# Kernel tuning notes

Hardware: AMD Instinct MI355X
Metric: run time of the kernel (lower is better)

## Reference

```python
import jax, jax.numpy as jnp
import numpy as np
import math

# Dims chosen per input_specs
B, Q, S, T = 8, 64, 64, 64          # batch, queries, stat (segment) count, tokens per segment
H, DH = 8, 64                        # heads, head dim
NH = H * DH                          # num_hiddens = 512
STAT_K, TOKEN_K = 8, 16
NEG = -1e6


def setup_inputs() -> dict:
    key = jax.random.key(0)
    ks = jax.random.split(key, 11)
    f = lambda k, sh: jax.random.normal(k, sh, dtype=jnp.float32)
    w = lambda k: f(k, (NH, NH)) * 0.05  # Linear weights stored as [in, out]
    return {
        "queries": f(ks[0], (B, Q, NH)),
        "stat_keys": f(ks[1], (B, S, NH)),
        "token_keys": f(ks[2], (B * S, T, NH)),
        "values": f(ks[3], (B * S, T, NH)),
        "stat_valid_lens": jax.random.randint(ks[4], (B,), 1, S + 1, dtype=jnp.int32),
        "Wq_stat": w(ks[5]),
        "Wq_token": w(ks[6]),
        "Wk_stat": w(ks[7]),
        "Wk_token": w(ks[8]),
        "Wv": w(ks[9]),
        "Wo": w(ks[10]),
    }


def reference(queries, stat_keys, token_keys, values, stat_valid_lens,
              Wq_stat, Wq_token, Wk_stat, Wk_token, Wv, Wo):
    scale = 1.0 / math.sqrt(DH)

    def split_heads(x):  # [b, L, H*DH] -> [b, H, L, DH]
        b, L, _ = x.shape
        return x.reshape(b, L, H, DH).transpose(0, 2, 1, 3)

    q_stat = split_heads(queries @ Wq_stat)        # [B,H,Q,DH]
    q_tok = split_heads(queries @ Wq_token)        # [B,H,Q,DH]
    k_stat = split_heads(stat_keys @ Wk_stat)      # [B,H,S,DH]
    # token_keys/values come in as [B*S, T, size]; per-head layout [B,H,S,T,DH]
    k_tok = (token_keys @ Wk_token).reshape(B, S, T, H, DH).transpose(0, 3, 1, 2, 4)
    v = (values @ Wv).reshape(B, S, T, H, DH).transpose(0, 3, 1, 2, 4)

    # --- stat-level scores, valid-length mask, top-k sparsification, softmax ---
    stat_scores = jnp.einsum('bhqd,bhsd->bhqs', q_stat, k_stat) * scale  # [B,H,Q,S]
    valid = jnp.arange(S)[None, None, None, :] < stat_valid_lens[:, None, None, None]
    stat_scores = jnp.where(valid, stat_scores, NEG)
    k1 = min(S - 1, STAT_K)
    _, top_idx = jax.lax.top_k(stat_scores, k1)                           # [B,H,Q,k1]
    keep = jax.nn.one_hot(top_idx, S, dtype=stat_scores.dtype).sum(-2) > 0  # [B,H,Q,S]
    stat_w = jax.nn.softmax(jnp.where(keep, stat_scores, NEG), axis=-1)   # [B,H,Q,S]

    # --- token-level scores. NOTE: the original code computes torch.topk but then
    # overwrites with the LAST k2 positions (token_weights[:, :, -k2:] = ...), so the
    # token top-k result is dead code; we faithfully reproduce the last-k2 masking. ---
    tok_scores = jnp.einsum('bhqd,bhstd->bhsqt', q_tok, k_tok) * scale    # [B,H,S,Q,T]
    k2 = min(T - 1, TOKEN_K)
    last_mask = jnp.arange(T) >= (T - k2)
    tok_w = jax.nn.softmax(jnp.where(last_mask, tok_scores, NEG), axis=-1)
    tok_w = tok_w.transpose(0, 1, 3, 2, 4)                                # [B,H,Q,S,T]

    # --- combine hierarchy and attend over values ---
    comb = stat_w[..., None] * tok_w                                      # [B,H,Q,S,T]
    out = jnp.einsum('bhqst,bhstd->bhqd', comb, v)                        # [B,H,Q,DH]
    out = out.transpose(0, 2, 1, 3).reshape(B, Q, NH)
    return out @ Wo
```

## Files before the change

### kernel.cpp

```cpp
#include <hip/hip_runtime.h>
#include <hip/hip_bf16.h>

#define BB 8
#define QQ 64
#define SS 64
#define TT 64
#define HH 8
#define DH 64
#define NHID 512
#define STAT_K 8
#define TOKEN_K 16

typedef short bf16x8 __attribute__((ext_vector_type(8)));
typedef float f32x4 __attribute__((ext_vector_type(4)));

__device__ inline ushort f2bf_rne(float x) {
    union { float f; unsigned u; } v; v.f = x;
    unsigned r = v.u + 0x7fff + ((v.u >> 16) & 1);
    return (ushort)(r >> 16);
}
__device__ inline float bf2f(ushort h) {
    union { unsigned u; float f; } v; v.u = ((unsigned)h) << 16;
    return v.f;
}

__global__ __launch_bounds__(256) void conv_w(
    const float* w0, const float* w1, const float* w2,
    const float* w3, const float* w4, const float* w5, ushort* wT)
{
    const int z = blockIdx.z;
    const float* srcs[6] = {w0, w1, w2, w3, w4, w5};
    const float* src = srcs[z];
    ushort* hi = wT + (size_t)z * 524288;
    ushort* lo = hi + 262144;
    __shared__ float t[32][33];
    const int c0 = blockIdx.x * 32, r0 = blockIdx.y * 32;
    const int tx = threadIdx.x & 31, ty = threadIdx.x >> 5;
    #pragma unroll
    for (int i = 0; i < 4; ++i)
        t[ty + 8 * i][tx] = src[(r0 + ty + 8 * i) * 512 + c0 + tx];
    __syncthreads();
    #pragma unroll
    for (int i = 0; i < 4; ++i) {
        float x = t[tx][ty + 8 * i];
        ushort h = f2bf_rne(x);
        int o = (c0 + ty + 8 * i) * 512 + r0 + tx;
        hi[o] = h;
        lo[o] = f2bf_rne(x - bf2f(h));
    }
}

__global__ __launch_bounds__(256) void gemm_split3(
    const float* __restrict__ queries, const float* __restrict__ stat_keys,
    const ushort* __restrict__ wT,
    float* __restrict__ q_stat, float* __restrict__ k_stat,
    float* __restrict__ q_tokf)
{
    const int z = blockIdx.z;
    const float* Afp = (z == 1) ? stat_keys : queries;
    const ushort* Bh = wT + (size_t)z * 524288;
    const ushort* Bl = Bh + 262144;
    float* C = (z == 0) ? q_stat : (z == 1) ? k_stat : q_tokf;
    const int K = 512, N = 512;

    __shared__ ushort As[2][64][40];
    __shared__ ushort Bs[2][64][40];
    const int tid = threadIdx.x;
    const int row0 = blockIdx.y * 64, col0 = blockIdx.x * 64;
    const int wave = tid >> 6, lane = tid & 63;
    const int wm = wave & 1, wn = wave >> 1;
    const int m16 = lane & 15, quad = lane >> 4;
    const int srow = tid >> 2, schunk = tid & 3;

    const float*  aptr  = Afp + (size_t)(row0 + srow) * K + schunk * 8;
    const ushort* bptrh = Bh + (size_t)(col0 + srow) * K + schunk * 8;
    const ushort* bptrl = Bl + (size_t)(col0 + srow) * K + schunk * 8;

    f32x4 acc[2][2];
    #pragma unroll
    for (int i = 0; i < 2; ++i)
        #pragma unroll
        for (int j = 0; j < 2; ++j)
            #pragma unroll
            for (int r = 0; r < 4; ++r) acc[i][j][r] = 0.f;

    for (int k0 = 0; k0 < K; k0 += 32) {
        float4 ax0 = ((const float4*)(aptr + k0))[0];
        float4 ax1 = ((const float4*)(aptr + k0))[1];
        uint4  bvh = *(const uint4*)(bptrh + k0);
        uint4  bvl = *(const uint4*)(bptrl + k0);
        ushort4 h0, h1, l0, l1;
        h0.x = f2bf_rne(ax0.x); l0.x = f2bf_rne(ax0.x - bf2f(h0.x));
        h0.y = f2bf_rne(ax0.y); l0.y = f2bf_rne(ax0.y - bf2f(h0.y));
        h0.z = f2bf_rne(ax0.z); l0.z = f2bf_rne(ax0.z - bf2f(h0.z));
        h0.w = f2bf_rne(ax0.w); l0.w = f2bf_rne(ax0.w - bf2f(h0.w));
        h1.x = f2bf_rne(ax1.x); l1.x = f2bf_rne(ax1.x - bf2f(h1.x));
        h1.y = f2bf_rne(ax1.y); l1.y = f2bf_rne(ax1.y - bf2f(h1.y));
        h1.z = f2bf_rne(ax1.z); l1.z = f2bf_rne(ax1.z - bf2f(h1.z));
        h1.w = f2bf_rne(ax1.w); l1.w = f2bf_rne(ax1.w - bf2f(h1.w));
        *(ushort4*)&As[0][srow][schunk * 8]     = h0;
        *(ushort4*)&As[0][srow][schunk * 8 + 4] = h1;
        *(ushort4*)&As[1][srow][schunk * 8]     = l0;
        *(ushort4*)&As[1][srow][schunk * 8 + 4] = l1;
        *(uint4*)&Bs[0][srow][schunk * 8] = bvh;
        *(uint4*)&Bs[1][srow][schunk * 8] = bvl;
        __syncthreads();

        bf16x8 af[2], bf[2], afl[2], bfl[2];
        #pragma unroll
        for (int i = 0; i < 2; ++i) {
            af[i]  = *(const bf16x8*)&As[0][wm * 32 + i * 16 + m16][quad * 8];
            bf[i]  = *(const bf16x8*)&Bs[0][wn * 32 + i * 16 + m16][quad * 8];
            afl[i] = *(const bf16x8*)&As[1][wm * 32 + i * 16 + m16][quad * 8];
            bfl[i] = *(const bf16x8*)&Bs[1][wn * 32 + i * 16 + m16][quad * 8];
        }
        #pragma unroll
        for (int i = 0; i < 2; ++i)
            #pragma unroll
            for (int j = 0; j < 2; ++j) {
                acc[i][j] = __builtin_amdgcn_mfma_f32_16x16x32_bf16(af[i], bf[j], acc[i][j], 0, 0, 0);
                acc[i][j] = __builtin_amdgcn_mfma_f32_16x16x32_bf16(af[i], bfl[j], acc[i][j], 0, 0, 0);
                acc[i][j] = __builtin_amdgcn_mfma_f32_16x16x32_bf16(afl[i], bf[j], acc[i][j], 0, 0, 0);
            }
        __syncthreads();
    }

    #pragma unroll
    for (int i = 0; i < 2; ++i)
        #pragma unroll
        for (int j = 0; j < 2; ++j) {
            int r0 = row0 + wm * 32 + i * 16 + quad * 4;
            int c = col0 + wn * 32 + j * 16 + m16;
            #pragma unroll
            for (int reg = 0; reg < 4; ++reg)
                C[(size_t)(r0 + reg) * N + c] = acc[i][j][reg];
        }
}

__global__ __launch_bounds__(256) void gemm_out(
    const ushort* __restrict__ Ah, const ushort* __restrict__ Al,
    const ushort* __restrict__ Bh, const ushort* __restrict__ Bl,
    float* __restrict__ C)
{
    const int K = 512, N = 512;
    __shared__ ushort As[2][64][40];
    __shared__ ushort Bs[2][64][40];
    const int tid = threadIdx.x;
    const int row0 = blockIdx.y * 64, col0 = blockIdx.x * 64;
    const int wave = tid >> 6, lane = tid & 63;
    const int wm = wave & 1, wn = wave >> 1;
    const int m16 = lane & 15, quad = lane >> 4;
    const int srow = tid >> 2, schunk = tid & 3;

    f32x4 acc[2][2];
    #pragma unroll
    for (int i = 0; i < 2; ++i)
        #pragma unroll
        for (int j = 0; j < 2; ++j)
            #pragma unroll
            for (int r = 0; r < 4; ++r) acc[i][j][r] = 0.f;

    for (int k0 = 0; k0 < K; k0 += 32) {
        const size_t aoff = (size_t)(row0 + srow) * K + k0 + schunk * 8;
        const size_t boff = (size_t)(col0 + srow) * K + k0 + schunk * 8;
        *(uint4*)&As[0][srow][schunk * 8] = *(const uint4*)(Ah + aoff);
        *(uint4*)&Bs[0][srow][schunk * 8] = *(const uint4*)(Bh + boff);
        *(uint4*)&As[1][srow][schunk * 8] = *(const uint4*)(Al + aoff);
        *(uint4*)&Bs[1][srow][schunk * 8] = *(const uint4*)(Bl + boff);
        __syncthreads();

        bf16x8 af[2], bf[2], afl[2], bfl[2];
        #pragma unroll
        for (int i = 0; i < 2; ++i) {
            af[i]  = *(const bf16x8*)&As[0][wm * 32 + i * 16 + m16][quad * 8];
            bf[i]  = *(const bf16x8*)&Bs[0][wn * 32 + i * 16 + m16][quad * 8];
            afl[i] = *(const bf16x8*)&As[1][wm * 32 + i * 16 + m16][quad * 8];
            bfl[i] = *(const bf16x8*)&Bs[1][wn * 32 + i * 16 + m16][quad * 8];
        }
        #pragma unroll
        for (int i = 0; i < 2; ++i)
            #pragma unroll
            for (int j = 0; j < 2; ++j) {
                acc[i][j] = __builtin_amdgcn_mfma_f32_16x16x32_bf16(af[i], bf[j], acc[i][j], 0, 0, 0);
                acc[i][j] = __builtin_amdgcn_mfma_f32_16x16x32_bf16(af[i], bfl[j], acc[i][j], 0, 0, 0);
                acc[i][j] = __builtin_amdgcn_mfma_f32_16x16x32_bf16(afl[i], bf[j], acc[i][j], 0, 0, 0);
            }
        __syncthreads();
    }

    #pragma unroll
    for (int i = 0; i < 2; ++i)
        #pragma unroll
        for (int j = 0; j < 2; ++j) {
            int r0 = row0 + wm * 32 + i * 16 + quad * 4;
            int c = col0 + wn * 32 + j * 16 + m16;
            #pragma unroll
            for (int reg = 0; reg < 4; ++reg)
                C[(size_t)(r0 + reg) * N + c] = acc[i][j][reg];
        }
}

__global__ __launch_bounds__(256) void gemm_tok(
    const float* __restrict__ token_keys, const ushort* __restrict__ wkt_h,
    ushort* __restrict__ k_tok)
{
    const int K = 512, N = 512;
    __shared__ ushort As[64][40];
    __shared__ ushort Bs[256][40];
    const int tid = threadIdx.x;
    const int row0 = blockIdx.y * 64, col0 = blockIdx.x * 256;
    const int wave = tid >> 6, lane = tid & 63;
    const int m16 = lane & 15, quad = lane >> 4;
    const int srow = tid >> 2, schunk = tid & 3;

    const int r = row0 + srow;
    const size_t arow = (size_t)((r >> 4) * 64 + 48 + (r & 15)) * K;

    f32x4 acc[4][4];
    #pragma unroll
    for (int i = 0; i < 4; ++i)
        #pragma unroll
        for (int j = 0; j < 4; ++j)
            #pragma unroll
            for (int rr = 0; rr < 4; ++rr) acc[i][j][rr] = 0.f;

    for (int k0 = 0; k0 < K; k0 += 32) {
        const float* ap = token_keys + arow + k0 + schunk * 8;
        float4 x0 = ((const float4*)ap)[0];
        float4 x1 = ((const float4*)ap)[1];
        ushort4 h0, h1;
        h0.x = f2bf_rne(x0.x); h0.y = f2bf_rne(x0.y);
        h0.z = f2bf_rne(x0.z); h0.w = f2bf_rne(x0.w);
        h1.x = f2bf_rne(x1.x); h1.y = f2bf_rne(x1.y);
        h1.z = f2bf_rne(x1.z); h1.w = f2bf_rne(x1.w);
        *(ushort4*)&As[srow][schunk * 8] = h0;
        *(ushort4*)&As[srow][schunk * 8 + 4] = h1;
        #pragma unroll
        for (int i = 0; i < 4; ++i) {
            int v = tid + i * 256;
            int brow = v >> 2, bchunk = v & 3;
            *(uint4*)&Bs[brow][bchunk * 8] =
                *(const uint4*)(wkt_h + (size_t)(col0 + brow) * K + k0 + bchunk * 8);
        }
        __syncthreads();

        bf16x8 af[4], bf[4];
        #pragma unroll
        for (int i = 0; i < 4; ++i) {
            af[i] = *(const bf16x8*)&As[i * 16 + m16][quad * 8];
            bf[i] = *(const bf16x8*)&Bs[wave * 64 + i * 16 + m16][quad * 8];
        }
        #pragma unroll
        for (int i = 0; i < 4; ++i)
            #pragma unroll
            for (int j = 0; j < 4; ++j)
                acc[i][j] = __builtin_amdgcn_mfma_f32_16x16x32_bf16(af[i], bf[j], acc[i][j], 0, 0, 0);
        __syncthreads();
    }

    #pragma unroll
    for (int i = 0; i < 4; ++i)
        #pragma unroll
        for (int j = 0; j < 4; ++j) {
            int r0 = row0 + i * 16 + quad * 4;
            int c = col0 + wave * 64 + j * 16 + m16;
            #pragma unroll
            for (int reg = 0; reg < 4; ++reg)
                k_tok[(size_t)(r0 + reg) * N + c] = f2bf_rne(acc[i][j][reg]);
        }
}

__global__ __launch_bounds__(256) void gemm_vT(
    const float* __restrict__ values, const ushort* __restrict__ wv_h,
    ushort* __restrict__ vT)
{
    const int K = 512;
    __shared__ ushort As[256][40];
    __shared__ ushort Bs[64][40];
    const int tid = threadIdx.x;
    const int row0m = blockIdx.y * 256, col0n = blockIdx.x * 64;
    const int wave = tid >> 6, lane = tid & 63;
    const int m16 = lane & 15, quad = lane >> 4;
    const int srow = tid >> 2, schunk = tid & 3;

    const int n = col0n + srow;
    const size_t brow = (size_t)((n >> 4) * 64 + 48 + (n & 15)) * K;

    f32x4 acc[4][4];
    #pragma unroll
    for (int i = 0; i < 4; ++i)
        #pragma unroll
        for (int j = 0; j < 4; ++j)
            #pragma unroll
            for (int rr = 0; rr < 4; ++rr) acc[i][j][rr] = 0.f;

    for (int k0 = 0; k0 < K; k0 += 32) {
        const float* bp = values + brow + k0 + schunk * 8;
        float4 x0 = ((const float4*)bp)[0];
        float4 x1 = ((const float4*)bp)[1];
        ushort4 h0, h1;
        h0.x = f2bf_rne(x0.x); h0.y = f2bf_rne(x0.y);
        h0.z = f2bf_rne(x0.z); h0.w = f2bf_rne(x0.w);
        h1.x = f2bf_rne(x1.x); h1.y = f2bf_rne(x1.y);
        h1.z = f2bf_rne(x1.z); h1.w = f2bf_rne(x1.w);
        *(ushort4*)&Bs[srow][schunk * 8] = h0;
        *(ushort4*)&Bs[srow][schunk * 8 + 4] = h1;
        #pragma unroll
        for (int i = 0; i < 4; ++i) {
            int v = tid + i * 256;
            int ar = v >> 2, ac = v & 3;
            *(uint4*)&As[ar][ac * 8] =
                *(const uint4*)(wv_h + (size_t)(row0m + ar) * K + k0 + ac * 8);
        }
        __syncthreads();

        bf16x8 af[4], bf[4];
        #pragma unroll
        for (int i = 0; i < 4; ++i) {
            af[i] = *(const bf16x8*)&As[wave * 64 + i * 16 + m16][quad * 8];
            bf[i] = *(const bf16x8*)&Bs[i * 16 + m16][quad * 8];
        }
        #pragma unroll
        for (int i = 0; i < 4; ++i)
            #pragma unroll
            for (int j = 0; j < 4; ++j)
                acc[i][j] = __builtin_amdgcn_mfma_f32_16x16x32_bf16(af[i], bf[j], acc[i][j], 0, 0, 0);
        __syncthreads();
    }

    #pragma unroll
    for (int i = 0; i < 4; ++i)
        #pragma unroll
        for (int j = 0; j < 4; ++j) {
            int m = row0m + wave * 64 + i * 16 + quad * 4;
            int c = col0n + j * 16 + m16;
            #pragma unroll
            for (int reg = 0; reg < 4; ++reg)
                vT[(size_t)(m + reg) * 8192 + c] = f2bf_rne(acc[i][j][reg]);
        }
}

__global__ __launch_bounds__(256) void attend_mfma(
    const float* __restrict__ q_stat, const float* __restrict__ k_stat,
    const float* __restrict__ q_tokf, const ushort* __restrict__ k_tok,
    const ushort* __restrict__ vT, const int* __restrict__ valid_lens,
    ushort* __restrict__ ctx_hi, ushort* __restrict__ ctx_lo)
{
    const int wg = blockIdx.x;
    const int b = wg >> 5, h = (wg >> 2) & 7, qt = wg & 3;
    const int tid = threadIdx.x, wave = tid >> 6, lane = tid & 63;
    const int m16 = lane & 15, quad = lane >> 4;

    __shared__ float  sQs[16][64];
    __shared__ ushort sQt[2][16][72];
    __shared__ float  sW[16][64];
    __shared__ ushort sKt[128][72];
    __shared__ ushort sCb[2][16][520];

    {
        int row = tid >> 4, c4 = tid & 15;
        const size_t qrow = (size_t)(b * 64 + qt * 16 + row) * 512 + h * 64;
        float4 xs = *(const float4*)(q_stat + qrow + c4 * 4);
        *(float4*)&sQs[row][c4 * 4] = xs;
        float4 xt = *(const float4*)(q_tokf + qrow + c4 * 4);
        ushort4 hh, ll;
        hh.x = f2bf_rne(xt.x); ll.x = f2bf_rne(xt.x - bf2f(hh.x));
        hh.y = f2bf_rne(xt.y); ll.y = f2bf_rne(xt.y - bf2f(hh.y));
        hh.z = f2bf_rne(xt.z); ll.z = f2bf_rne(xt.z - bf2f(hh.z));
        hh.w = f2bf_rne(xt.w); ll.w = f2bf_rne(xt.w - bf2f(hh.w));
        *(ushort4*)&sQt[0][row][c4 * 4] = hh;
        *(ushort4*)&sQt[1][row][c4 * 4] = ll;
    }
    __syncthreads();

    bf16x8 aQh[2], aQl[2];
    #pragma unroll
    for (int ks = 0; ks < 2; ++ks) {
        aQh[ks] = *(const bf16x8*)&sQt[0][m16][ks * 32 + quad * 8];
        aQl[ks] = *(const bf16x8*)&sQt[1][m16][ks * 32 + quad * 8];
    }

    const int vlen = valid_lens[b];
    for (int qq = 0; qq < 4; ++qq) {
        const int q = wave * 4 + qq;
        const float4* kr = (const float4*)(k_stat + (size_t)(b * SS + lane) * NHID + h * DH);
        const float4* sq4 = (const float4*)&sQs[q][0];
        float sc = 0.f;
        #pragma unroll
        for (int i = 0; i < 16; ++i) {
            float4 a = sq4[i], kk = kr[i];
            sc += a.x * kk.x + a.y * kk.y + a.z * kk.z + a.w * kk.w;
        }
        sc *= 0.125f;
        if (lane >= vlen) sc = -1e6f;

        float my = sc;
        float mv[STAT_K]; int mi[STAT_K];
        #pragma unroll
        for (int j = 0; j < STAT_K; ++j) {
            float v = my; int idx = lane;
            #pragma unroll
            for (int off = 32; off > 0; off >>= 1) {
                float ov = __shfl_down(v, off);
                int   oi = __shfl_down(idx, off);
                if (ov > v || (ov == v && oi < idx)) { v = ov; idx = oi; }
            }
            v = __shfl(v, 0); idx = __shfl(idx, 0);
            mv[j] = v; mi[j] = idx;
            if (lane == idx) my = -3e38f;
        }
        float m0 = mv[0], den = 0.f, w[STAT_K];
        #pragma unroll
        for (int j = 0; j < STAT_K; ++j) { w[j] = __expf(mv[j] - m0); den += w[j]; }
        float inv = 1.f / den;
        float wl = 0.f;
        #pragma unroll
        for (int j = 0; j < STAT_K; ++j)
            if (lane == mi[j]) wl = w[j] * inv;
        sW[q][lane] = wl;
    }

    f32x4 oacc;
    #pragma unroll
    for (int r = 0; r < 4; ++r) oacc[r] = 0.f;

    const ushort* vrow = vT + (size_t)(h * 64 + wave * 16 + m16) * 8192
                            + (size_t)b * 1024 + quad * 8;

    for (int half = 0; half < 2; ++half) {
        for (int g = 0; g < 4; ++g) {
            __syncthreads();
            {
                const ushort* base = k_tok
                    + (size_t)(b * 1024 + half * 512 + g * 128) * 512 + h * 64;
                #pragma unroll
                for (int i = 0; i < 4; ++i) {
                    int idx = i * 256 + tid;
                    int row = idx >> 3, ch = idx & 7;
                    *(uint4*)&sKt[row][ch * 8] =
                        *(const uint4*)(base + (size_t)row * 512 + ch * 8);
                }
            }
            __syncthreads();

            #pragma unroll
            for (int ti = 0; ti < 2; ++ti) {
                const int sl = wave * 2 + ti;
                const int sg = half * 32 + g * 8 + sl;
                bf16x8 b0 = *(const bf16x8*)&sKt[sl * 16 + m16][quad * 8];
                bf16x8 b1 = *(const bf16x8*)&sKt[sl * 16 + m16][32 + quad * 8];
                f32x4 c;
                #pragma unroll
                for (int r = 0; r < 4; ++r) c[r] = 0.f;
                c = __builtin_amdgcn_mfma_f32_16x16x32_bf16(aQh[0], b0, c, 0, 0, 0);
                c = __builtin_amdgcn_mfma_f32_16x16x32_bf16(aQl[0], b0, c, 0, 0, 0);
                c = __builtin_amdgcn_mfma_f32_16x16x32_bf16(aQh[1], b1, c, 0, 0, 0);
                c = __builtin_amdgcn_mfma_f32_16x16x32_bf16(aQl[1], b1, c, 0, 0, 0);

                const int klb = (g * 8 + sl) * 16 + m16;
                #pragma unroll
                for (int r = 0; r < 4; ++r) {
                    float v = c[r] * 0.125f;
                    float m = v;
                    m = fmaxf(m, __shfl_xor(m, 1));
                    m = fmaxf(m, __shfl_xor(m, 2));
                    m = fmaxf(m, __shfl_xor(m, 4));
                    m = fmaxf(m, __shfl_xor(m, 8));
                    float e = __expf(v - m);
                    float s = e;
                    s += __shfl_xor(s, 1);
                    s += __shfl_xor(s, 2);
                    s += __shfl_xor(s, 4);
                    s += __shfl_xor(s, 8);
                    float wt = (e / s) * sW[quad * 4 + r][sg];
                    ushort ch = f2bf_rne(wt);
                    sCb[0][quad * 4 + r][klb] = ch;
                    sCb[1][quad * 4 + r][klb] = f2bf_rne(wt - bf2f(ch));
                }
            }
        }
        __syncthreads();

        #pragma unroll
        for (int ks = 0; ks < 16; ++ks) {
            bf16x8 bv = *(const bf16x8*)(vrow + half * 512 + ks * 32);
            bf16x8 ah = *(const bf16x8*)&sCb[0][m16][ks * 32 + quad * 8];
            bf16x8 al = *(const bf16x8*)&sCb[1][m16][ks * 32 + quad * 8];
            oacc = __builtin_amdgcn_mfma_f32_16x16x32_bf16(ah, bv, oacc, 0, 0, 0);
            oacc = __builtin_amdgcn_mfma_f32_16x16x32_bf16(al, bv, oacc, 0, 0, 0);
        }
    }

    #pragma unroll
    for (int r = 0; r < 4; ++r) {
        const size_t o = (size_t)(b * 64 + qt * 16 + quad * 4 + r) * 512
                       + h * 64 + wave * 16 + m16;
        ushort hh = f2bf_rne(oacc[r]);
        ctx_hi[o] = hh;
        ctx_lo[o] = f2bf_rne(oacc[r] - bf2f(hh));
    }
}

extern "C" void kernel_launch(void* const* d_in, const int* in_sizes, int n_in,
                              void* d_out, int out_size, void* d_ws, size_t ws_size,
                              hipStream_t stream) {
    const float* queries    = (const float*)d_in[0];
    const float* stat_keys  = (const float*)d_in[1];
    const float* token_keys = (const float*)d_in[2];
    const float* values     = (const float*)d_in[3];
    const int*   valid_lens = (const int*)d_in[4];
    const float* Wq_stat    = (const float*)d_in[5];
    const float* Wq_token   = (const float*)d_in[6];
    const float* Wk_stat    = (const float*)d_in[7];
    const float* Wk_token   = (const float*)d_in[8];
    const float* Wv         = (const float*)d_in[9];
    const float* Wo         = (const float*)d_in[10];

    char* w = (char*)d_ws;
    ushort* wT      = (ushort*)(w + 0);
    float*  q_stat  = (float*)(w + 6291456);
    float*  k_stat  = (float*)(w + 7340032);
    float*  q_tokf  = (float*)(w + 8388608);
    ushort* k_tok   = (ushort*)(w + 9437184);
    ushort* vT      = (ushort*)(w + 17825792);
    ushort* ctx_hi  = (ushort*)(w + 26214400);
    ushort* ctx_lo  = ctx_hi + 262144;

    ushort* wkt_h = wT + 3 * 524288;
    ushort* wv_h  = wT + 4 * 524288;
    ushort* wo_h  = wT + 5 * 524288, *wo_l = wo_h + 262144;

    conv_w<<<dim3(16, 16, 6), 256, 0, stream>>>(
        Wq_stat, Wk_stat, Wq_token, Wk_token, Wv, Wo, wT);

    gemm_split3<<<dim3(8, 8, 3), 256, 0, stream>>>(
        queries, stat_keys, wT, q_stat, k_stat, q_tokf);

    gemm_tok<<<dim3(2, 128), 256, 0, stream>>>(token_keys, wkt_h, k_tok);

    gemm_vT<<<dim3(128, 2), 256, 0, stream>>>(values, wv_h, vT);

    attend_mfma<<<256, 256, 0, stream>>>(
        q_stat, k_stat, q_tokf, k_tok, vT, valid_lens, ctx_hi, ctx_lo);

    gemm_out<<<dim3(8, 8), 256, 0, stream>>>(
        ctx_hi, ctx_lo, wo_h, wo_l, (float*)d_out);
}
```

Baseline: 262.1 us.

## Merge token-key and value GEMMs into one launch; rank-based stat top-k

The separate k_tok and vT projection GEMMs become one kernel that picks its branch from blockIdx.z, so both run in a single 512-block launch instead of two sequential ones. In the attention kernel, the iterative 8-pass shuffle argmax top-k over stat scores is replaced by a shared-memory rank count: each lane counts how many scores beat its own and keeps itself if its rank is below STAT_K. The token-key tile is no longer staged in shared memory; each wave loads its K fragments straight from global, which removes per-group barriers but gives up LDS reuse and may raise global load latency.

```diff
diff --git a/kernel.cpp b/kernel.cpp
--- a/kernel.cpp
+++ b/kernel.cpp
@@ -200,22 +200,19 @@
         }
 }
 
-__global__ __launch_bounds__(256) void gemm_tok(
-    const float* __restrict__ token_keys, const ushort* __restrict__ wkt_h,
-    ushort* __restrict__ k_tok)
+__global__ __launch_bounds__(256) void gemm_tokv(
+    const float* __restrict__ token_keys, const float* __restrict__ values,
+    const ushort* __restrict__ wkt_h, const ushort* __restrict__ wv_h,
+    ushort* __restrict__ k_tok, ushort* __restrict__ vT)
 {
-    const int K = 512, N = 512;
-    __shared__ ushort As[64][40];
-    __shared__ ushort Bs[256][40];
+    const int K = 512;
+    __shared__ ushort sBig[256][40];
+    __shared__ ushort sSml[64][40];
     const int tid = threadIdx.x;
-    const int row0 = blockIdx.y * 64, col0 = blockIdx.x * 256;
     const int wave = tid >> 6, lane = tid & 63;
     const int m16 = lane & 15, quad = lane >> 4;
     const int srow = tid >> 2, schunk = tid & 3;
 
-    const int r = row0 + srow;
-    const size_t arow = (size_t)((r >> 4) * 64 + 48 + (r & 15)) * K;
-
     f32x4 acc[4][4];
     #pragma unroll
     for (int i = 0; i < 4; ++i)
@@ -224,120 +221,103 @@
             #pragma unroll
             for (int rr = 0; rr < 4; ++rr) acc[i][j][rr] = 0.f;
 
-    for (int k0 = 0; k0 < K; k0 += 32) {
-        const float* ap = token_keys + arow + k0 + schunk * 8;
-        float4 x0 = ((const float4*)ap)[0];
-        float4 x1 = ((const float4*)ap)[1];
-        ushort4 h0, h1;
-        h0.x = f2bf_rne(x0.x); h0.y = f2bf_rne(x0.y);
-        h0.z = f2bf_rne(x0.z); h0.w = f2bf_rne(x0.w);
-        h1.x = f2bf_rne(x1.x); h1.y = f2bf_rne(x1.y);
-        h1.z = f2bf_rne(x1.z); h1.w = f2bf_rne(x1.w);
-        *(ushort4*)&As[srow][schunk * 8] = h0;
-        *(ushort4*)&As[srow][schunk * 8 + 4] = h1;
-        #pragma unroll
-        for (int i = 0; i < 4; ++i) {
-            int v = tid + i * 256;
-            int brow = v >> 2, bchunk = v & 3;
-            *(uint4*)&Bs[brow][bchunk * 8] =
-                *(const uint4*)(wkt_h + (size_t)(col0 + brow) * K + k0 + bchunk * 8);
-        }
-        __syncthreads();
-
-        bf16x8 af[4], bf[4];
-        #pragma unroll
-        for (int i = 0; i < 4; ++i) {
-            af[i] = *(const bf16x8*)&As[i * 16 + m16][quad * 8];
-            bf[i] = *(const bf16x8*)&Bs[wave * 64 + i * 16 + m16][quad * 8];
-        }
+    if (blockIdx.z == 0) {
+        const int row0 = blockIdx.y * 64, col0 = blockIdx.x * 256;
+        const int r = row0 + srow;
+        const size_t arow = (size_t)((r >> 4) * 64 + 48 + (r & 15)) * K;
+
+        for (int k0 = 0; k0 < K; k0 += 32) {
+            const float* ap = token_keys + arow + k0 + schunk * 8;
+            float4 x0 = ((const float4*)ap)[0];
+            float4 x1 = ((const float4*)ap)[1];
+            ushort4 h0, h1;
+            h0.x = f2bf_rne(x0.x); h0.y = f2bf_rne(x0.y);
+            h0.z = f2bf_rne(x0.z); h0.w = f2bf_rne(x0.w);
+            h1.x = f2bf_rne(x1.x); h1.y = f2bf_rne(x1.y);
+            h1.z = f2bf_rne(x1.z); h1.w = f2bf_rne(x1.w);
+            *(ushort4*)&sSml[srow][schunk * 8] = h0;
+            *(ushort4*)&sSml[srow][schunk * 8 + 4] = h1;
+            #pragma unroll
+            for (int i = 0; i < 4; ++i) {
+                int v = tid + i * 256;
+                *(uint4*)&sBig[v >> 2][(v & 3) * 8] =
+                    *(const uint4*)(wkt_h + (size_t)(col0 + (v >> 2)) * K + k0 + (v & 3) * 8);
+            }
+            __syncthreads();
+
+            bf16x8 af[4], bf[4];
+            #pragma unroll
+            for (int i = 0; i < 4; ++i) {
+                af[i] = *(const bf16x8*)&sSml[i * 16 + m16][quad * 8];
+                bf[i] = *(const bf16x8*)&sBig[wave * 64 + i * 16 + m16][quad * 8];
+            }
+            #pragma unroll
+            for (int i = 0; i < 4; ++i)
+                #pragma unroll
+                for (int j = 0; j < 4; ++j)
+                    acc[i][j] = __builtin_amdgcn_mfma_f32_16x16x32_bf16(af[i], bf[j], acc[i][j], 0, 0, 0);
+            __syncthreads();
+        }
+
         #pragma unroll
         for (int i = 0; i < 4; ++i)
             #pragma unroll
-            for (int j = 0; j < 4; ++j)
-                acc[i][j] = __builtin_amdgcn_mfma_f32_16x16x32_bf16(af[i], bf[j], acc[i][j], 0, 0, 0);
-        __syncthreads();
-    }
-
-    #pragma unroll
-    for (int i = 0; i < 4; ++i)
-        #pragma unroll
-        for (int j = 0; j < 4; ++j) {
-            int r0 = row0 + i * 16 + quad * 4;
-            int c = col0 + wave * 64 + j * 16 + m16;
-            #pragma unroll
-            for (int reg = 0; reg < 4; ++reg)
-                k_tok[(size_t)(r0 + reg) * N + c] = f2bf_rne(acc[i][j][reg]);
-        }
-}
-
-__global__ __launch_bounds__(256) void gemm_vT(
-    const float* __restrict__ values, const ushort* __restrict__ wv_h,
-    ushort* __restrict__ vT)
-{
-    const int K = 512;
-    __shared__ ushort As[256][40];
-    __shared__ ushort Bs[64][40];
-    const int tid = threadIdx.x;
-    const int row0m = blockIdx.y * 256, col0n = blockIdx.x * 64;
-    const int wave = tid >> 6, lane = tid & 63;
-    const int m16 = lane & 15, quad = lane >> 4;
-    const int srow = tid >> 2, schunk = tid & 3;
-
-    const int n = col0n + srow;
-    const size_t brow = (size_t)((n >> 4) * 64 + 48 + (n & 15)) * K;
-
-    f32x4 acc[4][4];
-    #pragma unroll
-    for (int i = 0; i < 4; ++i)
-        #pragma unroll
-        for (int j = 0; j < 4; ++j)
-            #pragma unroll
-            for (int rr = 0; rr < 4; ++rr) acc[i][j][rr] = 0.f;
-
-    for (int k0 = 0; k0 < K; k0 += 32) {
-        const float* bp = values + brow + k0 + schunk * 8;
-        float4 x0 = ((const float4*)bp)[0];
-        float4 x1 = ((const float4*)bp)[1];
-        ushort4 h0, h1;
-        h0.x = f2bf_rne(x0.x); h0.y = f2bf_rne(x0.y);
-        h0.z = f2bf_rne(x0.z); h0.w = f2bf_rne(x0.w);
-        h1.x = f2bf_rne(x1.x); h1.y = f2bf_rne(x1.y);
-        h1.z = f2bf_rne(x1.z); h1.w = f2bf_rne(x1.w);
-        *(ushort4*)&Bs[srow][schunk * 8] = h0;
-        *(ushort4*)&Bs[srow][schunk * 8 + 4] = h1;
-        #pragma unroll
-        for (int i = 0; i < 4; ++i) {
-            int v = tid + i * 256;
-            int ar = v >> 2, ac = v & 3;
-            *(uint4*)&As[ar][ac * 8] =
-                *(const uint4*)(wv_h + (size_t)(row0m + ar) * K + k0 + ac * 8);
-        }
-        __syncthreads();
-
-        bf16x8 af[4], bf[4];
-        #pragma unroll
-        for (int i = 0; i < 4; ++i) {
-            af[i] = *(const bf16x8*)&As[wave * 64 + i * 16 + m16][quad * 8];
-            bf[i] = *(const bf16x8*)&Bs[i * 16 + m16][quad * 8];
-        }
+            for (int j = 0; j < 4; ++j) {
+                int r0 = row0 + i * 16 + quad * 4;
+                int c = col0 + wave * 64 + j * 16 + m16;
+                #pragma unroll
+                for (int reg = 0; reg < 4; ++reg)
+                    k_tok[(size_t)(r0 + reg) * 512 + c] = f2bf_rne(acc[i][j][reg]);
+            }
+    } else {
+        const int row0m = blockIdx.x * 256, col0n = blockIdx.y * 64;
+        const int n = col0n + srow;
+        const size_t brow = (size_t)((n >> 4) * 64 + 48 + (n & 15)) * K;
+
+        for (int k0 = 0; k0 < K; k0 += 32) {
+            const float* bp = values + brow + k0 + schunk * 8;
+            float4 x0 = ((const float4*)bp)[0];
+            float4 x1 = ((const float4*)bp)[1];
+            ushort4 h0, h1;
+            h0.x = f2bf_rne(x0.x); h0.y = f2bf_rne(x0.y);
+            h0.z = f2bf_rne(x0.z); h0.w = f2bf_rne(x0.w);
+            h1.x = f2bf_rne(x1.x); h1.y = f2bf_rne(x1.y);
+            h1.z = f2bf_rne(x1.z); h1.w = f2bf_rne(x1.w);
+            *(ushort4*)&sSml[srow][schunk * 8] = h0;
+            *(ushort4*)&sSml[srow][schunk * 8 + 4] = h1;
+            #pragma unroll
+            for (int i = 0; i < 4; ++i) {
+                int v = tid + i * 256;
+                *(uint4*)&sBig[v >> 2][(v & 3) * 8] =
+                    *(const uint4*)(wv_h + (size_t)(row0m + (v >> 2)) * K + k0 + (v & 3) * 8);
+            }
+            __syncthreads();
+
+            bf16x8 af[4], bf[4];
+            #pragma unroll
+            for (int i = 0; i < 4; ++i) {
+                af[i] = *(const bf16x8*)&sBig[wave * 64 + i * 16 + m16][quad * 8];
+                bf[i] = *(const bf16x8*)&sSml[i * 16 + m16][quad * 8];
+            }
+            #pragma unroll
+            for (int i = 0; i < 4; ++i)
+                #pragma unroll
+                for (int j = 0; j < 4; ++j)
+                    acc[i][j] = __builtin_amdgcn_mfma_f32_16x16x32_bf16(af[i], bf[j], acc[i][j], 0, 0, 0);
+            __syncthreads();
+        }
+
         #pragma unroll
         for (int i = 0; i < 4; ++i)
             #pragma unroll
-            for (int j = 0; j < 4; ++j)
-                acc[i][j] = __builtin_amdgcn_mfma_f32_16x16x32_bf16(af[i], bf[j], acc[i][j], 0, 0, 0);
-        __syncthreads();
-    }
-
-    #pragma unroll
-    for (int i = 0; i < 4; ++i)
-        #pragma unroll
-        for (int j = 0; j < 4; ++j) {
-            int m = row0m + wave * 64 + i * 16 + quad * 4;
-            int c = col0n + j * 16 + m16;
-            #pragma unroll
-            for (int reg = 0; reg < 4; ++reg)
-                vT[(size_t)(m + reg) * 8192 + c] = f2bf_rne(acc[i][j][reg]);
-        }
+            for (int j = 0; j < 4; ++j) {
+                int m = row0m + wave * 64 + i * 16 + quad * 4;
+                int c = col0n + j * 16 + m16;
+                #pragma unroll
+                for (int reg = 0; reg < 4; ++reg)
+                    vT[(size_t)(m + reg) * 8192 + c] = f2bf_rne(acc[i][j][reg]);
+            }
+    }
 }
 
 __global__ __launch_bounds__(256) void attend_mfma(
@@ -353,8 +333,8 @@
 
     __shared__ float  sQs[16][64];
     __shared__ ushort sQt[2][16][72];
+    __shared__ float  sSc[16][64];
     __shared__ float  sW[16][64];
-    __shared__ ushort sKt[128][72];
     __shared__ ushort sCb[2][16][520];
 
     {
@@ -381,6 +361,7 @@
     }
 
     const int vlen = valid_lens[b];
+    #pragma unroll
     for (int qq = 0; qq < 4; ++qq) {
         const int q = wave * 4 + qq;
         const float4* kr = (const float4*)(k_stat + (size_t)(b * SS + lane) * NHID + h * DH);
@@ -393,32 +374,34 @@
         }
         sc *= 0.125f;
         if (lane >= vlen) sc = -1e6f;
-
-        float my = sc;
-        float mv[STAT_K]; int mi[STAT_K];
-        #pragma unroll
-        for (int j = 0; j < STAT_K; ++j) {
-            float v = my; int idx = lane;
-            #pragma unroll
-            for (int off = 32; off > 0; off >>= 1) {
-                float ov = __shfl_down(v, off);
-                int   oi = __shfl_down(idx, off);
-                if (ov > v || (ov == v && oi < idx)) { v = ov; idx = oi; }
-            }
-            v = __shfl(v, 0); idx = __shfl(idx, 0);
-            mv[j] = v; mi[j] = idx;
-            if (lane == idx) my = -3e38f;
-        }
-        float m0 = mv[0], den = 0.f, w[STAT_K];
-        #pragma unroll
-        for (int j = 0; j < STAT_K; ++j) { w[j] = __expf(mv[j] - m0); den += w[j]; }
-        float inv = 1.f / den;
-        float wl = 0.f;
-        #pragma unroll
-        for (int j = 0; j < STAT_K; ++j)
-            if (lane == mi[j]) wl = w[j] * inv;
-        sW[q][lane] = wl;
-    }
+        sSc[q][lane] = sc;
+    }
+    __syncthreads();
+
+    #pragma unroll
+    for (int qq = 0; qq < 4; ++qq) {
+        const int q = wave * 4 + qq;
+        const float sc = sSc[q][lane];
+        const float4* row4 = (const float4*)&sSc[q][0];
+        int rank = 0;
+        float mx = -3e38f;
+        #pragma unroll
+        for (int i = 0; i < 16; ++i) {
+            float4 v = row4[i];
+            mx = fmaxf(mx, fmaxf(fmaxf(v.x, v.y), fmaxf(v.z, v.w)));
+            rank += (v.x > sc || (v.x == sc && (i * 4 + 0) < lane)) ? 1 : 0;
+            rank += (v.y > sc || (v.y == sc && (i * 4 + 1) < lane)) ? 1 : 0;
+            rank += (v.z > sc || (v.z == sc && (i * 4 + 2) < lane)) ? 1 : 0;
+            rank += (v.w > sc || (v.w == sc && (i * 4 + 3) < lane)) ? 1 : 0;
+        }
+        float e = (rank < STAT_K) ? __expf(sc - mx) : 0.f;
+        float s = e;
+        s += __shfl_xor(s, 1);  s += __shfl_xor(s, 2);
+        s += __shfl_xor(s, 4);  s += __shfl_xor(s, 8);
+        s += __shfl_xor(s, 16); s += __shfl_xor(s, 32);
+        sW[q][lane] = e / s;
+    }
+    __syncthreads();
 
     f32x4 oacc;
     #pragma unroll
@@ -428,55 +411,41 @@
                             + (size_t)b * 1024 + quad * 8;
 
     for (int half = 0; half < 2; ++half) {
-        for (int g = 0; g < 4; ++g) {
-            __syncthreads();
-            {
-                const ushort* base = k_tok
-                    + (size_t)(b * 1024 + half * 512 + g * 128) * 512 + h * 64;
-                #pragma unroll
-                for (int i = 0; i < 4; ++i) {
-                    int idx = i * 256 + tid;
-                    int row = idx >> 3, ch = idx & 7;
-                    *(uint4*)&sKt[row][ch * 8] =
-                        *(const uint4*)(base + (size_t)row * 512 + ch * 8);
-                }
-            }
-            __syncthreads();
-
-            #pragma unroll
-            for (int ti = 0; ti < 2; ++ti) {
-                const int sl = wave * 2 + ti;
-                const int sg = half * 32 + g * 8 + sl;
-                bf16x8 b0 = *(const bf16x8*)&sKt[sl * 16 + m16][quad * 8];
-                bf16x8 b1 = *(const bf16x8*)&sKt[sl * 16 + m16][32 + quad * 8];
-                f32x4 c;
-                #pragma unroll
-                for (int r = 0; r < 4; ++r) c[r] = 0.f;
-                c = __builtin_amdgcn_mfma_f32_16x16x32_bf16(aQh[0], b0, c, 0, 0, 0);
-                c = __builtin_amdgcn_mfma_f32_16x16x32_bf16(aQl[0], b0, c, 0, 0, 0);
-                c = __builtin_amdgcn_mfma_f32_16x16x32_bf16(aQh[1], b1, c, 0, 0, 0);
-                c = __builtin_amdgcn_mfma_f32_16x16x32_bf16(aQl[1], b1, c, 0, 0, 0);
-
-                const int klb = (g * 8 + sl) * 16 + m16;
-                #pragma unroll
-                for (int r = 0; r < 4; ++r) {
-                    float v = c[r] * 0.125f;
-                    float m = v;
-                    m = fmaxf(m, __shfl_xor(m, 1));
-                    m = fmaxf(m, __shfl_xor(m, 2));
-                    m = fmaxf(m, __shfl_xor(m, 4));
-                    m = fmaxf(m, __shfl_xor(m, 8));
-                    float e = __expf(v - m);
-                    float s = e;
-                    s += __shfl_xor(s, 1);
-                    s += __shfl_xor(s, 2);
-                    s += __shfl_xor(s, 4);
-                    s += __shfl_xor(s, 8);
-                    float wt = (e / s) * sW[quad * 4 + r][sg];
-                    ushort ch = f2bf_rne(wt);
-                    sCb[0][quad * 4 + r][klb] = ch;
-                    sCb[1][quad * 4 + r][klb] = f2bf_rne(wt - bf2f(ch));
-                }
+        #pragma unroll
+        for (int si = 0; si < 8; ++si) {
+            const int sl = wave * 8 + si;
+            const int sg = half * 32 + sl;
+            const ushort* kb = k_tok
+                + (size_t)(b * 1024 + sg * 16 + m16) * 512 + h * 64 + quad * 8;
+            bf16x8 b0 = *(const bf16x8*)kb;
+            bf16x8 b1 = *(const bf16x8*)(kb + 32);
+            f32x4 c;
+            #pragma unroll
+            for (int r = 0; r < 4; ++r) c[r] = 0.f;
+            c = __builtin_amdgcn_mfma_f32_16x16x32_bf16(aQh[0], b0, c, 0, 0, 0);
+            c = __builtin_amdgcn_mfma_f32_16x16x32_bf16(aQl[0], b0, c, 0, 0, 0);
+            c = __builtin_amdgcn_mfma_f32_16x16x32_bf16(aQh[1], b1, c, 0, 0, 0);
+            c = __builtin_amdgcn_mfma_f32_16x16x32_bf16(aQl[1], b1, c, 0, 0, 0);
+
+            const int klb = sl * 16 + m16;
+            #pragma unroll
+            for (int r = 0; r < 4; ++r) {
+                float v = c[r] * 0.125f;
+                float m = v;
+                m = fmaxf(m, __shfl_xor(m, 1));
+                m = fmaxf(m, __shfl_xor(m, 2));
+                m = fmaxf(m, __shfl_xor(m, 4));
+                m = fmaxf(m, __shfl_xor(m, 8));
+                float e = __expf(v - m);
+                float s = e;
+                s += __shfl_xor(s, 1);
+                s += __shfl_xor(s, 2);
+                s += __shfl_xor(s, 4);
+                s += __shfl_xor(s, 8);
+                float wt = (e / s) * sW[quad * 4 + r][sg];
+                ushort ch = f2bf_rne(wt);
+                sCb[0][quad * 4 + r][klb] = ch;
+                sCb[1][quad * 4 + r][klb] = f2bf_rne(wt - bf2f(ch));
             }
         }
         __syncthreads();
@@ -489,6 +458,7 @@
             oacc = __builtin_amdgcn_mfma_f32_16x16x32_bf16(ah, bv, oacc, 0, 0, 0);
             oacc = __builtin_amdgcn_mfma_f32_16x16x32_bf16(al, bv, oacc, 0, 0, 0);
         }
+        __syncthreads();
     }
 
     #pragma unroll
@@ -536,9 +506,8 @@
     gemm_split3<<<dim3(8, 8, 3), 256, 0, stream>>>(
         queries, stat_keys, wT, q_stat, k_stat, q_tokf);
 
-    gemm_tok<<<dim3(2, 128), 256, 0, stream>>>(token_keys, wkt_h, k_tok);
-
-    gemm_vT<<<dim3(128, 2), 256, 0, stream>>>(values, wv_h, vT);
+    gemm_tokv<<<dim3(2, 128, 2), 256, 0, stream>>>(
+        token_keys, values, wkt_h, wv_h, k_tok, vT);
 
     attend_mfma<<<256, 256, 0, stream>>>(
         q_stat, k_stat, q_tokf, k_tok, vT, valid_lens, ctx_hi, ctx_lo);
```

Measured after the change: 261.7 us. Within noise of the previous version (-0.2%).
